# Optimization experiments

Measured on AMD Instinct MI355X. Metric: run time of the kernel, lower is better.

## Reference

```python
import jax, jax.numpy as jnp
import numpy as np


def _normalize_adj(edge_index, num_nodes):
    # add self loops
    loop = jnp.arange(num_nodes, dtype=edge_index.dtype)
    row = jnp.concatenate([edge_index[0], loop])
    col = jnp.concatenate([edge_index[1], loop])
    deg = jax.ops.segment_sum(jnp.ones(row.shape[0], jnp.float32), row,
                              num_segments=num_nodes)
    dis = jnp.where(deg > 0, jax.lax.rsqrt(deg), 0.0)  # deg^{-1/2}, inf->0
    ew = dis[row] * dis[col]
    return row, col, ew


def _gcn_conv(x, W, b, row, col, ew, num_nodes):
    h = x @ W.T + b                       # dense linear [N, out]
    msg = h[col] * ew[:, None]            # gather + scale [E', out]
    return jax.ops.segment_sum(msg, row, num_segments=num_nodes)  # scatter_add


def setup_inputs() -> dict:
    N, E, IN, HID, OUT = 100000, 1600000, 128, 128, 64
    key = jax.random.key(0)
    k1, k2, k3, k4 = jax.random.split(key, 4)
    x = jax.random.normal(k1, (N, IN), jnp.float32)
    edge_index = jax.random.randint(k2, (2, E), 0, N, jnp.int64)
    # xavier_uniform for weights, zero bias (as in reset_parameters)
    lim1 = float(np.sqrt(6.0 / (IN + HID)))
    lim2 = float(np.sqrt(6.0 / (HID + OUT)))
    W1 = jax.random.uniform(k3, (HID, IN), jnp.float32, -lim1, lim1)
    b1 = jnp.zeros((HID,), jnp.float32)
    W2 = jax.random.uniform(k4, (OUT, HID), jnp.float32, -lim2, lim2)
    b2 = jnp.zeros((OUT,), jnp.float32)
    return {"x": x, "edge_index": edge_index, "num_nodes": N,
            "W1": W1, "b1": b1, "W2": W2, "b2": b2}


def reference(x, edge_index, num_nodes, W1, b1, W2, b2):
    row, col, ew = _normalize_adj(edge_index, num_nodes)
    h = _gcn_conv(x, W1, b1, row, col, ew, num_nodes)
    h = jax.nn.relu(h)  # dropout is identity in eval mode
    out = _gcn_conv(h, W2, b2, row, col, ew, num_nodes)
    return out
```

## Files before the change

kernel.cpp:

```cpp
#include <hip/hip_runtime.h>
#include <hip/hip_bf16.h>
#include <stdint.h>


#define TPB 256
#define NBLK_C 256
#define TPB_C 1024
#define MAX_NB 2048

typedef __attribute__((ext_vector_type(8))) __bf16 bf16x8;
typedef __attribute__((ext_vector_type(4))) float f32x4;

__device__ __forceinline__ float bf16lo(unsigned u) { return __uint_as_float(u << 16); }
__device__ __forceinline__ float bf16hi(unsigned u) { return __uint_as_float(u & 0xffff0000u); }
__device__ __forceinline__ unsigned short f2bf(float f) {
    unsigned u = __float_as_uint(f);
    return (unsigned short)((u + 0x7fff + ((u >> 16) & 1)) >> 16);
}

__global__ void detect64_kernel(const int* __restrict__ ei32, int* __restrict__ flag) {
    if (threadIdx.x == 0 && blockIdx.x == 0) {
        int is64 = 1;
        for (int t = 0; t < 64; ++t) {
            if (ei32[2 * t + 1] != 0) { is64 = 0; break; }
        }
        *flag = is64;
    }
}

__global__ __launch_bounds__(TPB_C) void hist_extract_kernel(const void* __restrict__ ei, int E,
                                                             int CH,
                                                             const int* __restrict__ flag,
                                                             int* __restrict__ row32,
                                                             int* __restrict__ col32,
                                                             int* __restrict__ hist,
                                                             int NB, int N) {
    __shared__ int h[MAX_NB];
    int tid = threadIdx.x;
    for (int bin = tid; bin < NB; bin += TPB_C) h[bin] = 0;
    __syncthreads();

    int b = blockIdx.x;
    int s = b * CH;
    int end = min(E, s + CH);
    int is64 = *flag;
    unsigned uN = (unsigned)N;
    if (is64) {
        const long long* p = (const long long*)ei;
        for (int e = s + tid; e < end; e += TPB_C) {
            int r = (int)p[e];
            int c = (int)p[E + e];
            row32[e] = r;
            col32[e] = c;
            if ((unsigned)r < uN && (unsigned)c < uN) atomicAdd(&h[r >> 7], 1);
        }
    } else {
        const int* p = (const int*)ei;
        for (int e = s + tid; e < end; e += TPB_C) {
            int r = p[e];
            int c = p[E + e];
            row32[e] = r;
            col32[e] = c;
            if ((unsigned)r < uN && (unsigned)c < uN) atomicAdd(&h[r >> 7], 1);
        }
    }
    __syncthreads();
    for (int bin = tid; bin < NB; bin += TPB_C) hist[bin * NBLK_C + b] = h[bin];
}

__global__ __launch_bounds__(NBLK_C) void colscan_kernel(int* __restrict__ hist,
                                                         int* __restrict__ binTotal) {
    __shared__ int sm[NBLK_C];
    int bin = blockIdx.x;
    int tid = threadIdx.x;
    int v = hist[bin * NBLK_C + tid];
    sm[tid] = v;
    __syncthreads();
    for (int o = 1; o < NBLK_C; o <<= 1) {
        int x = (tid >= o) ? sm[tid - o] : 0;
        __syncthreads();
        sm[tid] += x;
        __syncthreads();
    }
    hist[bin * NBLK_C + tid] = sm[tid] - v;
    if (tid == NBLK_C - 1) binTotal[bin] = sm[NBLK_C - 1];
}

__global__ __launch_bounds__(1024) void binscan_kernel(const int* __restrict__ binTotal,
                                                       int* __restrict__ bucketStart, int NB) {
    __shared__ int sm[1024];
    int tid = threadIdx.x;
    int v = (tid < NB) ? binTotal[tid] : 0;
    sm[tid] = v;
    __syncthreads();
    for (int o = 1; o < 1024; o <<= 1) {
        int x = (tid >= o) ? sm[tid - o] : 0;
        __syncthreads();
        sm[tid] += x;
        __syncthreads();
    }
    if (tid < NB) bucketStart[tid] = sm[tid] - v;
}

__global__ __launch_bounds__(TPB_C) void scatter_kernel(const int* __restrict__ row32,
                                                        const int* __restrict__ col32, int E,
                                                        int CH,
                                                        const int* __restrict__ hist,
                                                        const int* __restrict__ bucketStart,
                                                        int* __restrict__ bucketed,
                                                        int NB, int N) {
    __shared__ int cur[MAX_NB];
    int tid = threadIdx.x;
    int b = blockIdx.x;
    for (int bin = tid; bin < NB; bin += TPB_C)
        cur[bin] = bucketStart[bin] + hist[bin * NBLK_C + b];
    __syncthreads();

    int s = b * CH;
    int end = min(E, s + CH);
    unsigned uN = (unsigned)N;
    for (int e = s + tid; e < end; e += TPB_C) {
        int r = row32[e];
        int c = col32[e];
        if ((unsigned)r < uN && (unsigned)c < uN) {
            int pos = atomicAdd(&cur[r >> 7], 1);
            bucketed[pos] = (c << 7) | (r & 127);
        }
    }
}

__global__ __launch_bounds__(TPB) void finecsr_kernel(const int* __restrict__ bucketed,
                                                      const int* __restrict__ bucketStart,
                                                      const int* __restrict__ binTotal,
                                                      int* __restrict__ offs,
                                                      int* __restrict__ cnt,
                                                      float* __restrict__ dis,
                                                      int* __restrict__ csr, int N) {
    __shared__ int c128[128];
    __shared__ int cur128[128];
    __shared__ int sm[TPB];
    int bin = blockIdx.x;
    int tid = threadIdx.x;
    int s = bucketStart[bin];
    int m = binTotal[bin];

    if (tid < 128) c128[tid] = 0;
    __syncthreads();
    for (int i = tid; i < m; i += TPB) atomicAdd(&c128[bucketed[s + i] & 127], 1);
    __syncthreads();

    int v = (tid < 128) ? c128[tid] : 0;
    sm[tid] = v;
    __syncthreads();
    for (int o = 1; o < 128; o <<= 1) {
        int x = (tid >= o) ? sm[tid - o] : 0;
        __syncthreads();
        sm[tid] += x;
        __syncthreads();
    }
    if (tid < 128) {
        int excl = sm[tid] - v;
        int r = bin * 128 + tid;
        if (r < N) {
            offs[r] = s + excl;
            cnt[r] = v;
            dis[r] = rsqrtf((float)v + 1.0f);
        }
        cur128[tid] = s + excl;
    }
    __syncthreads();
    for (int i = tid; i < m; i += TPB) {
        int p = bucketed[s + i];
        int pos = atomicAdd(&cur128[p & 127], 1);
        csr[pos] = p >> 7;
    }
}

template <int BN, bool INB16>
__global__ __launch_bounds__(256, 2) void gemm_mfma_kernel(const void* __restrict__ Xp,
                                                           const float* __restrict__ W,
                                                           const float* __restrict__ bias,
                                                           const float* __restrict__ dis,
                                                           unsigned short* __restrict__ Hb,
                                                           int N) {
    constexpr int XST = 136;
    __shared__ unsigned short Xs[128 * XST];
    __shared__ unsigned short Ws[BN * XST];

    const int tid = threadIdx.x;
    const int r0 = blockIdx.x * 128;

    if (INB16) {
        const ushort4* Xv = (const ushort4*)Xp;
        for (int idx = tid; idx < 128 * 32; idx += 256) {
            int row = idx >> 5, q = idx & 31;
            int rg = r0 + row;
            if (rg >= N) rg = N - 1;
            *(ushort4*)&Xs[row * XST + q * 4] = Xv[(size_t)rg * 32 + q];
        }
    } else {
        const float4* Xv = (const float4*)Xp;
        for (int idx = tid; idx < 128 * 32; idx += 256) {
            int row = idx >> 5, q = idx & 31;
            int rg = r0 + row;
            if (rg >= N) rg = N - 1;
            float4 v = Xv[(size_t)rg * 32 + q];
            ushort4 s = make_ushort4(f2bf(v.x), f2bf(v.y), f2bf(v.z), f2bf(v.w));
            *(ushort4*)&Xs[row * XST + q * 4] = s;
        }
    }
    {
        const float4* Wv = (const float4*)W;
        for (int idx = tid; idx < BN * 32; idx += 256) {
            int n = idx >> 5, q = idx & 31;
            float4 v = Wv[n * 32 + q];
            ushort4 s = make_ushort4(f2bf(v.x), f2bf(v.y), f2bf(v.z), f2bf(v.w));
            *(ushort4*)&Ws[n * XST + q * 4] = s;
        }
    }
    __syncthreads();

    constexpr int RT = (BN == 128) ? 4 : 2;
    constexpr int CT = 4;
    const int wave = tid >> 6, lane = tid & 63;
    const int l15 = lane & 15, q8 = lane >> 4;
    const int row0 = (BN == 128) ? (wave & 1) * 64 : wave * 32;
    const int col0 = (BN == 128) ? (wave >> 1) * 64 : 0;

    f32x4 zero = {0.f, 0.f, 0.f, 0.f};
    f32x4 acc[RT][CT];
#pragma unroll
    for (int rt = 0; rt < RT; ++rt)
#pragma unroll
        for (int ct = 0; ct < CT; ++ct) acc[rt][ct] = zero;

#pragma unroll
    for (int ks = 0; ks < 4; ++ks) {
        int ko = ks * 32 + q8 * 8;
        bf16x8 a[RT], b[CT];
#pragma unroll
        for (int rt = 0; rt < RT; ++rt)
            a[rt] = *(const bf16x8*)&Xs[(row0 + rt * 16 + l15) * XST + ko];
#pragma unroll
        for (int ct = 0; ct < CT; ++ct)
            b[ct] = *(const bf16x8*)&Ws[(col0 + ct * 16 + l15) * XST + ko];
#pragma unroll
        for (int rt = 0; rt < RT; ++rt)
#pragma unroll
            for (int ct = 0; ct < CT; ++ct)
                acc[rt][ct] = __builtin_amdgcn_mfma_f32_16x16x32_bf16(
                    a[rt], b[ct], acc[rt][ct], 0, 0, 0);
    }

    float bv[CT];
#pragma unroll
    for (int ct = 0; ct < CT; ++ct) bv[ct] = bias[col0 + ct * 16 + l15];
#pragma unroll
    for (int rt = 0; rt < RT; ++rt)
#pragma unroll
        for (int r = 0; r < 4; ++r) {
            int row = r0 + row0 + rt * 16 + q8 * 4 + r;
            if (row < N) {
                float dn = dis[row];
#pragma unroll
                for (int ct = 0; ct < CT; ++ct)
                    Hb[(size_t)row * BN + col0 + ct * 16 + l15] =
                        f2bf((acc[rt][ct][r] + bv[ct]) * dn);
            }
        }
}

template <int F, bool RELU, bool OB16>
__global__ __launch_bounds__(TPB) void agg_kernel(const unsigned short* __restrict__ Hb,
                                                  const int* __restrict__ csr,
                                                  const int* __restrict__ offs,
                                                  const int* __restrict__ cnt,
                                                  const float* __restrict__ dis,
                                                  void* __restrict__ outp, int N) {
    constexpr int FPL = F / 16;
    constexpr int NW = FPL / 2;
    constexpr int RS = F / 2;

    int w = (blockIdx.x * TPB + threadIdx.x) >> 6;
    if (w >= N) return;
    int lane = threadIdx.x & 63;
    int g = lane >> 4;
    int fl = lane & 15;

    float di = dis[w];
    int s = offs[w];
    int d = cnt[w];

    const unsigned* Hu = (const unsigned*)Hb;

    float acc[FPL];
    {
        unsigned su[NW];
        if constexpr (NW == 4) {
            uint4 v = *(const uint4*)&Hu[(size_t)w * RS + fl * NW];
            su[0] = v.x; su[1] = v.y; su[2] = v.z; su[3] = v.w;
        } else {
            uint2 v = *(const uint2*)&Hu[(size_t)w * RS + fl * NW];
            su[0] = v.x; su[1] = v.y;
        }
        float sm = (g == 0) ? 1.0f : 0.0f;
#pragma unroll
        for (int t = 0; t < NW; ++t) {
            acc[2 * t] = sm * bf16lo(su[t]);
            acc[2 * t + 1] = sm * bf16hi(su[t]);
        }
    }

    for (int base = 0; base < d; base += 64) {
        int rem = d - base;
        if (rem > 64) rem = 64;
        int cl = (lane < rem) ? csr[s + base + lane] : 0;

        for (int e = 0; e < rem; e += 16) {
            int cc[4];
            float m[4];
#pragma unroll
            for (int k = 0; k < 4; ++k) {
                int idx = e + k * 4 + g;
                cc[k] = __shfl(cl, idx & 63);
                m[k] = (idx < rem) ? 1.0f : 0.0f;
            }
            unsigned u[4][NW];
#pragma unroll
            for (int k = 0; k < 4; ++k) {
                if constexpr (NW == 4) {
                    uint4 v = *(const uint4*)&Hu[(size_t)cc[k] * RS + fl * NW];
                    u[k][0] = v.x; u[k][1] = v.y; u[k][2] = v.z; u[k][3] = v.w;
                } else {
                    uint2 v = *(const uint2*)&Hu[(size_t)cc[k] * RS + fl * NW];
                    u[k][0] = v.x; u[k][1] = v.y;
                }
            }
#pragma unroll
            for (int k = 0; k < 4; ++k)
#pragma unroll
                for (int t = 0; t < NW; ++t) {
                    acc[2 * t]     = fmaf(m[k], bf16lo(u[k][t]), acc[2 * t]);
                    acc[2 * t + 1] = fmaf(m[k], bf16hi(u[k][t]), acc[2 * t + 1]);
                }
        }
    }

#pragma unroll
    for (int off = 16; off < 64; off <<= 1)
#pragma unroll
        for (int j = 0; j < FPL; ++j) acc[j] += __shfl_xor(acc[j], off);

#pragma unroll
    for (int j = 0; j < FPL; ++j) {
        acc[j] *= di;
        if (RELU) acc[j] = fmaxf(acc[j], 0.0f);
    }

    if (lane < 16) {
        if constexpr (OB16) {
            unsigned dw[NW];
#pragma unroll
            for (int t = 0; t < NW; ++t)
                dw[t] = (unsigned)f2bf(acc[2 * t]) | ((unsigned)f2bf(acc[2 * t + 1]) << 16);
            unsigned* op = (unsigned*)outp;
            if constexpr (NW == 4) {
                *(uint4*)&op[(size_t)w * RS + fl * NW] = make_uint4(dw[0], dw[1], dw[2], dw[3]);
            } else {
                *(uint2*)&op[(size_t)w * RS + fl * NW] = make_uint2(dw[0], dw[1]);
            }
        } else {
            float4* op = (float4*)outp;
            if constexpr (FPL == 4) {
                op[(size_t)w * 16 + fl] = make_float4(acc[0], acc[1], acc[2], acc[3]);
            } else {
                op[(size_t)w * 32 + fl * 2]     = make_float4(acc[0], acc[1], acc[2], acc[3]);
                op[(size_t)w * 32 + fl * 2 + 1] = make_float4(acc[4], acc[5], acc[6], acc[7]);
            }
        }
    }
}

extern "C" void kernel_launch(void* const* d_in, const int* in_sizes, int n_in,
                              void* d_out, int out_size, void* d_ws, size_t ws_size,
                              hipStream_t stream) {
    const float* x  = (const float*)d_in[0];
    const void*  ei = d_in[1];
    const float* W1 = (const float*)d_in[3];
    const float* b1 = (const float*)d_in[4];
    const float* W2 = (const float*)d_in[5];
    const float* b2 = (const float*)d_in[6];
    float* out = (float*)d_out;

    const int IN = 128, HID = 128;
    const int N = in_sizes[0] / IN;
    const int E = in_sizes[1] / 2;
    const int NB = (N + 127) >> 7;
    const int CH = (E + NBLK_C - 1) / NBLK_C;

    char* ws = (char*)d_ws;
    size_t off = 0;
    auto alloc = [&](size_t bytes) -> void* {
        void* p = (void*)(ws + off);
        off += (bytes + 255) & ~(size_t)255;
        return p;
    };
    int*   flag     = (int*)alloc(256);
    int*   cnt      = (int*)alloc((size_t)N * 4);
    int*   offs     = (int*)alloc((size_t)N * 4);
    float* dis      = (float*)alloc((size_t)N * 4);
    int*   row32    = (int*)alloc((size_t)E * 4);
    int*   col32    = (int*)alloc((size_t)E * 4);
    int*   bucketed = (int*)alloc((size_t)E * 4);
    int*   csr      = (int*)alloc((size_t)E * 4);
    int*   hist     = (int*)alloc((size_t)NB * NBLK_C * 4);
    int*   binTotal = (int*)alloc((size_t)NB * 4);
    int*   bStart   = (int*)alloc((size_t)NB * 4);
    unsigned short* H1b = (unsigned short*)alloc((size_t)N * HID * 2);
    unsigned short* R1b = (unsigned short*)alloc((size_t)N * HID * 2);
    unsigned short* H2b = H1b;

    detect64_kernel<<<1, 64, 0, stream>>>((const int*)ei, flag);

    hist_extract_kernel<<<NBLK_C, TPB_C, 0, stream>>>(ei, E, CH, flag, row32, col32,
                                                      hist, NB, N);
    colscan_kernel<<<NB, NBLK_C, 0, stream>>>(hist, binTotal);
    binscan_kernel<<<1, 1024, 0, stream>>>(binTotal, bStart, NB);
    scatter_kernel<<<NBLK_C, TPB_C, 0, stream>>>(row32, col32, E, CH, hist, bStart,
                                                 bucketed, NB, N);
    finecsr_kernel<<<NB, TPB, 0, stream>>>(bucketed, bStart, binTotal,
                                           offs, cnt, dis, csr, N);

    int ngrid = (N + 127) / 128;

    gemm_mfma_kernel<128, false><<<ngrid, 256, 0, stream>>>(x, W1, b1, dis, H1b, N);
    agg_kernel<128, true, true><<<(N + 3) / 4, TPB, 0, stream>>>(H1b, csr, offs, cnt,
                                                                 dis, R1b, N);

    gemm_mfma_kernel<64, true><<<ngrid, 256, 0, stream>>>(R1b, W2, b2, dis, H2b, N);
    agg_kernel<64, false, false><<<(N + 3) / 4, TPB, 0, stream>>>(H2b, csr, offs, cnt,
                                                                  dis, out, N);
}
```

Baseline: 282.8 us.

## Fold dtype detect and bin scan into neighbors; pad-row gathers with packed adds

Removes the separate 64-bit detection and bin-scan kernels. Detection moves into a wavefront ballot inside the histogram kernel, and the bin prefix sum is recomputed redundantly inside the scatter and fine-CSR kernels, cutting two launches and their serialization. The aggregation loop now processes 32 neighbors per iteration with two batches of loads in flight. Out-of-range lanes gather a zeroed pad row N instead of multiplying by a mask, and accumulation uses v_pk_add_f32. The cost is redundant scan work in every block, plus an extra pad row written by the GEMM kernel.

```diff
diff --git a/kernel.cpp b/kernel.cpp
--- a/kernel.cpp
+++ b/kernel.cpp
@@ -10,6 +10,7 @@
 
 typedef __attribute__((ext_vector_type(8))) __bf16 bf16x8;
 typedef __attribute__((ext_vector_type(4))) float f32x4;
+typedef __attribute__((ext_vector_type(2))) float f32x2;
 
 __device__ __forceinline__ float bf16lo(unsigned u) { return __uint_as_float(u << 16); }
 __device__ __forceinline__ float bf16hi(unsigned u) { return __uint_as_float(u & 0xffff0000u); }
@@ -17,33 +18,33 @@
     unsigned u = __float_as_uint(f);
     return (unsigned short)((u + 0x7fff + ((u >> 16) & 1)) >> 16);
 }
-
-__global__ void detect64_kernel(const int* __restrict__ ei32, int* __restrict__ flag) {
-    if (threadIdx.x == 0 && blockIdx.x == 0) {
-        int is64 = 1;
-        for (int t = 0; t < 64; ++t) {
-            if (ei32[2 * t + 1] != 0) { is64 = 0; break; }
-        }
-        *flag = is64;
-    }
+__device__ __forceinline__ f32x2 pk_add(f32x2 a, f32x2 b) {
+    f32x2 d;
+    asm("v_pk_add_f32 %0, %1, %2" : "=v"(d) : "v"(a), "v"(b));
+    return d;
 }
 
 __global__ __launch_bounds__(TPB_C) void hist_extract_kernel(const void* __restrict__ ei, int E,
                                                              int CH,
-                                                             const int* __restrict__ flag,
                                                              int* __restrict__ row32,
                                                              int* __restrict__ col32,
                                                              int* __restrict__ hist,
                                                              int NB, int N) {
     __shared__ int h[MAX_NB];
+    __shared__ int s_is64;
     int tid = threadIdx.x;
+    if (tid < 64) {
+        int x = ((const int*)ei)[2 * tid + 1];
+        unsigned long long b = __ballot(x != 0);
+        if (tid == 0) s_is64 = (b == 0ull);
+    }
     for (int bin = tid; bin < NB; bin += TPB_C) h[bin] = 0;
     __syncthreads();
 
     int b = blockIdx.x;
     int s = b * CH;
     int end = min(E, s + CH);
-    int is64 = *flag;
+    int is64 = s_is64;
     unsigned uN = (unsigned)N;
     if (is64) {
         const long long* p = (const long long*)ei;
@@ -86,34 +87,28 @@
     if (tid == NBLK_C - 1) binTotal[bin] = sm[NBLK_C - 1];
 }
 
-__global__ __launch_bounds__(1024) void binscan_kernel(const int* __restrict__ binTotal,
-                                                       int* __restrict__ bucketStart, int NB) {
-    __shared__ int sm[1024];
-    int tid = threadIdx.x;
-    int v = (tid < NB) ? binTotal[tid] : 0;
-    sm[tid] = v;
-    __syncthreads();
-    for (int o = 1; o < 1024; o <<= 1) {
-        int x = (tid >= o) ? sm[tid - o] : 0;
-        __syncthreads();
-        sm[tid] += x;
-        __syncthreads();
-    }
-    if (tid < NB) bucketStart[tid] = sm[tid] - v;
-}
-
 __global__ __launch_bounds__(TPB_C) void scatter_kernel(const int* __restrict__ row32,
                                                         const int* __restrict__ col32, int E,
                                                         int CH,
                                                         const int* __restrict__ hist,
-                                                        const int* __restrict__ bucketStart,
+                                                        const int* __restrict__ binTotal,
                                                         int* __restrict__ bucketed,
                                                         int NB, int N) {
     __shared__ int cur[MAX_NB];
+    __shared__ int sm2[TPB_C];
     int tid = threadIdx.x;
     int b = blockIdx.x;
-    for (int bin = tid; bin < NB; bin += TPB_C)
-        cur[bin] = bucketStart[bin] + hist[bin * NBLK_C + b];
+
+    int v = (tid < NB) ? binTotal[tid] : 0;
+    sm2[tid] = v;
+    __syncthreads();
+    for (int o = 1; o < TPB_C; o <<= 1) {
+        int x = (tid >= o) ? sm2[tid - o] : 0;
+        __syncthreads();
+        sm2[tid] += x;
+        __syncthreads();
+    }
+    if (tid < NB) cur[tid] = (sm2[tid] - v) + hist[tid * NBLK_C + b];
     __syncthreads();
 
     int s = b * CH;
@@ -130,7 +125,6 @@
 }
 
 __global__ __launch_bounds__(TPB) void finecsr_kernel(const int* __restrict__ bucketed,
-                                                      const int* __restrict__ bucketStart,
                                                       const int* __restrict__ binTotal,
                                                       int* __restrict__ offs,
                                                       int* __restrict__ cnt,
@@ -139,9 +133,19 @@
     __shared__ int c128[128];
     __shared__ int cur128[128];
     __shared__ int sm[TPB];
+    __shared__ int red[TPB];
     int bin = blockIdx.x;
     int tid = threadIdx.x;
-    int s = bucketStart[bin];
+
+    int part = 0;
+    for (int i = tid; i < bin; i += TPB) part += binTotal[i];
+    red[tid] = part;
+    __syncthreads();
+    for (int o = TPB / 2; o > 0; o >>= 1) {
+        if (tid < o) red[tid] += red[tid + o];
+        __syncthreads();
+    }
+    int s = red[0];
     int m = binTotal[bin];
 
     if (tid < 128) c128[tid] = 0;
@@ -190,6 +194,9 @@
     const int tid = threadIdx.x;
     const int r0 = blockIdx.x * 128;
 
+    if (blockIdx.x == 0 && tid < (BN >> 1))
+        ((unsigned*)Hb)[(size_t)N * (BN >> 1) + tid] = 0u;
+
     if (INB16) {
         const ushort4* Xv = (const ushort4*)Xp;
         for (int idx = tid; idx < 128 * 32; idx += 256) {
@@ -293,22 +300,33 @@
 
     const unsigned* Hu = (const unsigned*)Hb;
 
-    float acc[FPL];
-    {
+    f32x2 acc2[NW];
+#pragma unroll
+    for (int t = 0; t < NW; ++t) acc2[t] = (f32x2){0.f, 0.f};
+
+    auto accum_row = [&](const unsigned (&u)[NW]) {
+#pragma unroll
+        for (int t = 0; t < NW; ++t) {
+            f32x2 lh;
+            lh.x = bf16lo(u[t]);
+            lh.y = bf16hi(u[t]);
+            acc2[t] = pk_add(acc2[t], lh);
+        }
+    };
+    auto load_row = [&](unsigned (&u)[NW], int r) {
+        if constexpr (NW == 4) {
+            uint4 v = *(const uint4*)(Hu + (size_t)r * RS + fl * NW);
+            u[0] = v.x; u[1] = v.y; u[2] = v.z; u[3] = v.w;
+        } else {
+            uint2 v = *(const uint2*)(Hu + (size_t)r * RS + fl * NW);
+            u[0] = v.x; u[1] = v.y;
+        }
+    };
+
+    if (g == 0) {
         unsigned su[NW];
-        if constexpr (NW == 4) {
-            uint4 v = *(const uint4*)&Hu[(size_t)w * RS + fl * NW];
-            su[0] = v.x; su[1] = v.y; su[2] = v.z; su[3] = v.w;
-        } else {
-            uint2 v = *(const uint2*)&Hu[(size_t)w * RS + fl * NW];
-            su[0] = v.x; su[1] = v.y;
-        }
-        float sm = (g == 0) ? 1.0f : 0.0f;
-#pragma unroll
-        for (int t = 0; t < NW; ++t) {
-            acc[2 * t] = sm * bf16lo(su[t]);
-            acc[2 * t + 1] = sm * bf16hi(su[t]);
-        }
+        load_row(su, w);
+        accum_row(su);
     }
 
     for (int base = 0; base < d; base += 64) {
@@ -316,45 +334,56 @@
         if (rem > 64) rem = 64;
         int cl = (lane < rem) ? csr[s + base + lane] : 0;
 
-        for (int e = 0; e < rem; e += 16) {
-            int cc[4];
-            float m[4];
+        for (int e = 0; e < rem; e += 32) {
+            int cc0[4];
 #pragma unroll
             for (int k = 0; k < 4; ++k) {
                 int idx = e + k * 4 + g;
-                cc[k] = __shfl(cl, idx & 63);
-                m[k] = (idx < rem) ? 1.0f : 0.0f;
-            }
-            unsigned u[4][NW];
-#pragma unroll
-            for (int k = 0; k < 4; ++k) {
-                if constexpr (NW == 4) {
-                    uint4 v = *(const uint4*)&Hu[(size_t)cc[k] * RS + fl * NW];
-                    u[k][0] = v.x; u[k][1] = v.y; u[k][2] = v.z; u[k][3] = v.w;
-                } else {
-                    uint2 v = *(const uint2*)&Hu[(size_t)cc[k] * RS + fl * NW];
-                    u[k][0] = v.x; u[k][1] = v.y;
+                int raw = __shfl(cl, idx & 63);
+                cc0[k] = (idx < rem) ? raw : N;
+            }
+            unsigned u0[4][NW];
+#pragma unroll
+            for (int k = 0; k < 4; ++k) load_row(u0[k], cc0[k]);
+
+            const bool two = (e + 16) < rem;
+            int cc1[4];
+            unsigned u1[4][NW];
+            if (two) {
+#pragma unroll
+                for (int k = 0; k < 4; ++k) {
+                    int idx = e + 16 + k * 4 + g;
+                    int raw = __shfl(cl, idx & 63);
+                    cc1[k] = (idx < rem) ? raw : N;
                 }
-            }
-#pragma unroll
-            for (int k = 0; k < 4; ++k)
-#pragma unroll
-                for (int t = 0; t < NW; ++t) {
-                    acc[2 * t]     = fmaf(m[k], bf16lo(u[k][t]), acc[2 * t]);
-                    acc[2 * t + 1] = fmaf(m[k], bf16hi(u[k][t]), acc[2 * t + 1]);
-                }
+#pragma unroll
+                for (int k = 0; k < 4; ++k) load_row(u1[k], cc1[k]);
+            }
+#pragma unroll
+            for (int k = 0; k < 4; ++k) accum_row(u0[k]);
+            if (two) {
+#pragma unroll
+                for (int k = 0; k < 4; ++k) accum_row(u1[k]);
+            }
         }
     }
 
 #pragma unroll
     for (int off = 16; off < 64; off <<= 1)
 #pragma unroll
-        for (int j = 0; j < FPL; ++j) acc[j] += __shfl_xor(acc[j], off);
-
-#pragma unroll
-    for (int j = 0; j < FPL; ++j) {
-        acc[j] *= di;
-        if (RELU) acc[j] = fmaxf(acc[j], 0.0f);
+        for (int t = 0; t < NW; ++t) {
+            acc2[t].x += __shfl_xor(acc2[t].x, off);
+            acc2[t].y += __shfl_xor(acc2[t].y, off);
+        }
+
+#pragma unroll
+    for (int t = 0; t < NW; ++t) {
+        acc2[t].x *= di;
+        acc2[t].y *= di;
+        if (RELU) {
+            acc2[t].x = fmaxf(acc2[t].x, 0.0f);
+            acc2[t].y = fmaxf(acc2[t].y, 0.0f);
+        }
     }
 
     if (lane < 16) {
@@ -362,7 +391,7 @@
             unsigned dw[NW];
 #pragma unroll
             for (int t = 0; t < NW; ++t)
-                dw[t] = (unsigned)f2bf(acc[2 * t]) | ((unsigned)f2bf(acc[2 * t + 1]) << 16);
+                dw[t] = (unsigned)f2bf(acc2[t].x) | ((unsigned)f2bf(acc2[t].y) << 16);
             unsigned* op = (unsigned*)outp;
             if constexpr (NW == 4) {
                 *(uint4*)&op[(size_t)w * RS + fl * NW] = make_uint4(dw[0], dw[1], dw[2], dw[3]);
@@ -371,11 +400,14 @@
             }
         } else {
             float4* op = (float4*)outp;
-            if constexpr (FPL == 4) {
-                op[(size_t)w * 16 + fl] = make_float4(acc[0], acc[1], acc[2], acc[3]);
+            if constexpr (NW == 2) {
+                op[(size_t)w * 16 + fl] =
+                    make_float4(acc2[0].x, acc2[0].y, acc2[1].x, acc2[1].y);
             } else {
-                op[(size_t)w * 32 + fl * 2]     = make_float4(acc[0], acc[1], acc[2], acc[3]);
-                op[(size_t)w * 32 + fl * 2 + 1] = make_float4(acc[4], acc[5], acc[6], acc[7]);
+                op[(size_t)w * 32 + fl * 2] =
+                    make_float4(acc2[0].x, acc2[0].y, acc2[1].x, acc2[1].y);
+                op[(size_t)w * 32 + fl * 2 + 1] =
+                    make_float4(acc2[2].x, acc2[2].y, acc2[3].x, acc2[3].y);
             }
         }
     }
@@ -405,7 +437,6 @@
         off += (bytes + 255) & ~(size_t)255;
         return p;
     };
-    int*   flag     = (int*)alloc(256);
     int*   cnt      = (int*)alloc((size_t)N * 4);
     int*   offs     = (int*)alloc((size_t)N * 4);
     float* dis      = (float*)alloc((size_t)N * 4);
@@ -415,21 +446,16 @@
     int*   csr      = (int*)alloc((size_t)E * 4);
     int*   hist     = (int*)alloc((size_t)NB * NBLK_C * 4);
     int*   binTotal = (int*)alloc((size_t)NB * 4);
-    int*   bStart   = (int*)alloc((size_t)NB * 4);
-    unsigned short* H1b = (unsigned short*)alloc((size_t)N * HID * 2);
-    unsigned short* R1b = (unsigned short*)alloc((size_t)N * HID * 2);
+    unsigned short* H1b = (unsigned short*)alloc((size_t)(N + 1) * HID * 2);
+    unsigned short* R1b = (unsigned short*)alloc((size_t)(N + 1) * HID * 2);
     unsigned short* H2b = H1b;
 
-    detect64_kernel<<<1, 64, 0, stream>>>((const int*)ei, flag);
-
-    hist_extract_kernel<<<NBLK_C, TPB_C, 0, stream>>>(ei, E, CH, flag, row32, col32,
+    hist_extract_kernel<<<NBLK_C, TPB_C, 0, stream>>>(ei, E, CH, row32, col32,
                                                       hist, NB, N);
     colscan_kernel<<<NB, NBLK_C, 0, stream>>>(hist, binTotal);
-    binscan_kernel<<<1, 1024, 0, stream>>>(binTotal, bStart, NB);
-    scatter_kernel<<<NBLK_C, TPB_C, 0, stream>>>(row32, col32, E, CH, hist, bStart,
+    scatter_kernel<<<NBLK_C, TPB_C, 0, stream>>>(row32, col32, E, CH, hist, binTotal,
                                                  bucketed, NB, N);
-    finecsr_kernel<<<NB, TPB, 0, stream>>>(bucketed, bStart, binTotal,
-                                           offs, cnt, dis, csr, N);
+    finecsr_kernel<<<NB, TPB, 0, stream>>>(bucketed, binTotal, offs, cnt, dis, csr, N);
 
     int ngrid = (N + 127) / 128;
 
```

New measurement: 274.3 us. 1.03x faster.
